# Performance work log

Measured on AMD Instinct MI355X. Metric: run time of the kernel, lower is better.

Reference implementation:

```python
import jax, jax.numpy as jnp
import numpy as np

SENT_LEN = 8192
C = 1024  # class_num


def setup_inputs() -> dict:
    key = jax.random.key(0)
    k1, k2 = jax.random.split(key)
    scores = jax.random.normal(k1, (SENT_LEN, C), dtype=jnp.float32)
    T = jax.random.normal(k2, (C, C), dtype=jnp.float32)  # transition params (random_weights=True)
    return {"scores": scores, "T": T}


def reference(scores, T):
    """Log-domain marginals of a first-order linear-chain CRF.

    alpha[i, j] = scores[i, j] + LSE_k(alpha[i-1, k] + T[k, j])
    beta[i, j]  = scores[i, j] + LSE_k(T[j, k] + beta[i+1, k])
    marginals   = alpha + beta - scores - Z,  Z = LSE(alpha[-1])
    (alpha+beta double-counts scores[i], hence the subtraction.)
    """
    def alpha_step(a_prev, s):
        # a_prev: [C] ; broadcast-add against T then logsumexp over source class k
        a = s + jax.nn.logsumexp(a_prev[:, None] + T, axis=0)
        return a, a

    a0 = scores[0]
    _, alpha_rest = jax.lax.scan(alpha_step, a0, scores[1:])
    alpha = jnp.concatenate([a0[None], alpha_rest], axis=0)  # [N, C]

    def beta_step(b_next, s):
        b = s + jax.nn.logsumexp(T + b_next[None, :], axis=1)
        return b, b

    bN = scores[-1]
    _, beta_rest = jax.lax.scan(beta_step, bN, scores[:-1], reverse=True)
    beta = jnp.concatenate([beta_rest, bN[None]], axis=0)  # [N, C]

    Z = jax.nn.logsumexp(alpha[-1])  # partition function (log)
    return alpha + beta - scores - Z
```

## Files before the change

### kernel.cpp

```cpp
#include <hip/hip_runtime.h>
#include <stdint.h>
#include <float.h>


#define NR    8192
#define CC    1024
#define SEGR  4
#define GH    4
#define NSEG  2048
#define TPB   1024
#define NWV   16
#define G     16
#define NBLK  256
#define MAXT  (GH + SEGR - 1)
#define SHIFT 6.0f

typedef _Float16 f16x8 __attribute__((ext_vector_type(8)));
typedef float    f32x4 __attribute__((ext_vector_type(4)));
typedef __fp16   hv2   __attribute__((ext_vector_type(2)));

__device__ __forceinline__ uint32_t packw(float a, float b) {
  hv2 r = __builtin_amdgcn_cvt_pkrtz(a, b);
  return __builtin_bit_cast(uint32_t, r);
}

__global__ __launch_bounds__(256) void crf_pack(
    const float* __restrict__ T, uint4* __restrict__ Ef, uint4* __restrict__ Eb)
{
  const int bid = blockIdx.x;
  const int dir = bid >> 9;
  const int tid = threadIdx.x;
  const int fid = ((bid & 511) << 2) + (tid >> 6);
  const int lane = tid & 63;
  const int kt = fid >> 6, ntg = fid & 63;
  const int q = lane >> 4, li = lane & 15;
  const int n = ntg * 16 + li;
  const int kb = kt * 32 + q * 8;
  uint32_t o[4];
  if (dir == 0) {
#pragma unroll
    for (int p = 0; p < 4; ++p) {
      const float e0 = __expf(T[(size_t)(kb + 2 * p) * CC + n] - SHIFT);
      const float e1 = __expf(T[(size_t)(kb + 2 * p + 1) * CC + n] - SHIFT);
      o[p] = packw(e0, e1);
    }
    Ef[(size_t)fid * 64 + lane] = make_uint4(o[0], o[1], o[2], o[3]);
  } else {
    const float4 t0 = *(const float4*)&T[(size_t)n * CC + kb];
    const float4 t1 = *(const float4*)&T[(size_t)n * CC + kb + 4];
    o[0] = packw(__expf(t0.x - SHIFT), __expf(t0.y - SHIFT));
    o[1] = packw(__expf(t0.z - SHIFT), __expf(t0.w - SHIFT));
    o[2] = packw(__expf(t1.x - SHIFT), __expf(t1.y - SHIFT));
    o[3] = packw(__expf(t1.z - SHIFT), __expf(t1.w - SHIFT));
    Eb[(size_t)fid * 64 + lane] = make_uint4(o[0], o[1], o[2], o[3]);
  }
}

__global__ __launch_bounds__(TPB) void crf_seg(
    const float* __restrict__ scores,
    const uint4* __restrict__ Ef, const uint4* __restrict__ Eb,
    float* __restrict__ out, float* __restrict__ qrows,
    double* __restrict__ OA, double* __restrict__ OB,
    double* __restrict__ eLf, double* __restrict__ gLf,
    double* __restrict__ eLb, double* __restrict__ gLb, int useQ)
{
  __shared__ unsigned short wh[G][CC + 8];
  __shared__ float mgw[G][NWV + 1];
  __shared__ float lsw[G][NWV + 1];

  const int bid  = blockIdx.x;
  const int xcd  = bid & 7;
  const bool fwd = (xcd < 4);
  const int q    = (xcd & 3) * 32 + (bid >> 3);
  const int tid  = threadIdx.x;
  const int wv   = tid >> 6;
  const int lane = tid & 63;
  const int quad = lane >> 4, li = lane & 15;
  const int wbase = wv * 64;
  const int rot  = (bid >> 3) & 31;

  const uint4*  E    = fwd ? Ef : Eb;
  float*        emit = fwd ? out : qrows;
  double*       Oarr = fwd ? OA : OB;
  double*       eL   = fwd ? eLf : eLb;
  double*       gL   = fwd ? gLf : gLb;

  auto geom = [&](int c, int& g0, int& tE, int& tend) {
    const int s = G * q + c;
    if (fwd) {
      const int f = SEGR * s;
      const int gg = (f - GH) > 0 ? (f - GH) : 0;
      g0 = gg; tE = f - gg; tend = f + SEGR - 1 - gg;
    } else {
      const int h = NR - 1 - SEGR * s;
      const int gg = (h + GH) < (NR - 1) ? (h + GH) : (NR - 1);
      g0 = gg; tE = gg - h; tend = tE + SEGR - 1;
    }
  };

  float pub[4][4];
#pragma unroll
  for (int reg = 0; reg < 4; ++reg) {
    int g0, tE, tend; geom(quad * 4 + reg, g0, tE, tend);
    const size_t rb = (size_t)g0 * CC;
#pragma unroll
    for (int nt = 0; nt < 4; ++nt)
      pub[nt][reg] = scores[rb + wbase + nt * 16 + li];
  }
  double Off = 0.0;
#pragma unroll
  for (int reg = 0; reg < 4; ++reg) {
    int g0, tE, tend; geom(quad * 4 + reg, g0, tE, tend);
    if (tE == 0) {
      const size_t rb = (size_t)g0 * CC;
#pragma unroll
      for (int nt = 0; nt < 4; ++nt) {
        const int j = wbase + nt * 16 + li;
        const float v = fwd ? 0.f : pub[nt][reg];
        if (useQ) emit[rb + j] = v;
        else if (!fwd) atomicAdd(&out[rb + j], v);
      }
    }
  }
  if (tid < G) {
    int g0, tE, tend; geom(tid, g0, tE, tend);
    if (tE == 0) Oarr[g0] = 0.0;
  }

  const uint4* Eln = E + lane;

  for (int t = 1; t <= MAXT; ++t) {
    float sc[4][4] = {};
#pragma unroll
    for (int reg = 0; reg < 4; ++reg) {
      int g0, tE, tend; geom(quad * 4 + reg, g0, tE, tend);
      if (t <= tend) {
        const size_t rb = (size_t)(fwd ? g0 + t : g0 - t) * CC;
#pragma unroll
        for (int nt = 0; nt < 4; ++nt)
          sc[nt][reg] = scores[rb + wbase + nt * 16 + li];
      }
    }

#pragma unroll
    for (int reg = 0; reg < 4; ++reg) {
      float m = pub[0][reg];
#pragma unroll
      for (int nt = 1; nt < 4; ++nt) m = fmaxf(m, pub[nt][reg]);
      m = fmaxf(m, __shfl_xor(m, 1, 64));
      m = fmaxf(m, __shfl_xor(m, 2, 64));
      m = fmaxf(m, __shfl_xor(m, 4, 64));
      m = fmaxf(m, __shfl_xor(m, 8, 64));
      if (li == 0) mgw[quad * 4 + reg][wv] = m;
    }
    __syncthreads();
    float mgli = mgw[li][0];
#pragma unroll
    for (int w = 1; w < NWV; ++w) mgli = fmaxf(mgli, mgw[li][w]);
    float mg4[4];
#pragma unroll
    for (int reg = 0; reg < 4; ++reg) mg4[reg] = __shfl(mgli, quad * 4 + reg, 64);
    if (tid < G) Off += (double)mgli;

    bool bstep = false;
#pragma unroll
    for (int c = 0; c < G; ++c) {
      int g0, tE, tend; geom(c, g0, tE, tend);
      bstep = bstep || (t == tE && tE > 0) || (t - 1 == tend);
    }
    if (bstep) {
#pragma unroll
      for (int reg = 0; reg < 4; ++reg) {
        float s = 0.f;
#pragma unroll
        for (int nt = 0; nt < 4; ++nt) s += __expf(pub[nt][reg] - mg4[reg]);
        s += __shfl_xor(s, 1, 64);
        s += __shfl_xor(s, 2, 64);
        s += __shfl_xor(s, 4, 64);
        s += __shfl_xor(s, 8, 64);
        if (li == 0) lsw[quad * 4 + reg][wv] = s;
      }
    }

#pragma unroll
    for (int reg = 0; reg < 4; ++reg) {
      const int row = quad * 4 + reg;
#pragma unroll
      for (int nt = 0; nt < 4; ++nt) {
        const __fp16 h = (__fp16)__expf(pub[nt][reg] - mg4[reg]);
        wh[row][wbase + nt * 16 + li] = __builtin_bit_cast(unsigned short, h);
      }
    }
    __syncthreads();

    if (bstep && tid < G) {
      float s = lsw[tid][0];
#pragma unroll
      for (int w = 1; w < NWV; ++w) s += lsw[tid][w];
      const double L = (double)__logf(s) + Off;
      int g0, tE, tend; geom(tid, g0, tE, tend);
      if (t == tE && tE > 0) gL[G * q + tid] = L;
      if (t - 1 == tend)     eL[G * q + tid] = L;
    }

    f32x4 acc[4];
#pragma unroll
    for (int nt = 0; nt < 4; ++nt) acc[nt] = (f32x4){0.f, 0.f, 0.f, 0.f};
#pragma unroll 2
    for (int kt = 0; kt < 32; ++kt) {
      const int ktr = (kt + rot) & 31;
      const uint4 a4 = *(const uint4*)&wh[li][ktr * 32 + quad * 8];
      const f16x8 af = __builtin_bit_cast(f16x8, a4);
#pragma unroll
      for (int nt = 0; nt < 4; ++nt) {
        const uint4 b4 = Eln[(size_t)(ktr * 64 + wv * 4 + nt) * 64];
        acc[nt] = __builtin_amdgcn_mfma_f32_16x16x32_f16(
            af, __builtin_bit_cast(f16x8, b4), acc[nt], 0, 0, 0);
      }
    }

#pragma unroll
    for (int reg = 0; reg < 4; ++reg) {
      int g0, tE, tend; geom(quad * 4 + reg, g0, tE, tend);
      if (t <= tend) {
        const size_t rb = (size_t)(fwd ? g0 + t : g0 - t) * CC;
        const bool em = (t >= tE);
#pragma unroll
        for (int nt = 0; nt < 4; ++nt) {
          const float pv = sc[nt][reg] + SHIFT + __logf(acc[nt][reg]);
          pub[nt][reg] = pv;
          if (em) {
            const int j = wbase + nt * 16 + li;
            const float ov = fwd ? (pv - sc[nt][reg]) : pv;
            if (useQ) emit[rb + j] = ov;
            else atomicAdd(&out[rb + j], ov);
          }
        }
      }
    }
    if (tid < G) {
      int g0, tE, tend; geom(tid, g0, tE, tend);
      if (t >= tE && t <= tend) Oarr[fwd ? g0 + t : g0 - t] = Off;
    }
  }

  {
#pragma unroll
    for (int reg = 0; reg < 4; ++reg) {
      float m = pub[0][reg];
#pragma unroll
      for (int nt = 1; nt < 4; ++nt) m = fmaxf(m, pub[nt][reg]);
      m = fmaxf(m, __shfl_xor(m, 1, 64));
      m = fmaxf(m, __shfl_xor(m, 2, 64));
      m = fmaxf(m, __shfl_xor(m, 4, 64));
      m = fmaxf(m, __shfl_xor(m, 8, 64));
      if (li == 0) mgw[quad * 4 + reg][wv] = m;
    }
    __syncthreads();
    float mgli = mgw[li][0];
#pragma unroll
    for (int w = 1; w < NWV; ++w) mgli = fmaxf(mgli, mgw[li][w]);
    float mg4[4];
#pragma unroll
    for (int reg = 0; reg < 4; ++reg) mg4[reg] = __shfl(mgli, quad * 4 + reg, 64);
    if (tid < G) Off += (double)mgli;
#pragma unroll
    for (int reg = 0; reg < 4; ++reg) {
      float s = 0.f;
#pragma unroll
      for (int nt = 0; nt < 4; ++nt) s += __expf(pub[nt][reg] - mg4[reg]);
      s += __shfl_xor(s, 1, 64);
      s += __shfl_xor(s, 2, 64);
      s += __shfl_xor(s, 4, 64);
      s += __shfl_xor(s, 8, 64);
      if (li == 0) lsw[quad * 4 + reg][wv] = s;
    }
    __syncthreads();
    if (tid < G) {
      int g0, tE, tend; geom(tid, g0, tE, tend);
      if (tend == MAXT) {
        float s = lsw[tid][0];
#pragma unroll
        for (int w = 1; w < NWV; ++w) s += lsw[tid][w];
        eL[G * q + tid] = (double)__logf(s) + Off;
      }
    }
  }
}

__global__ __launch_bounds__(128) void crf_stitch(
    const double* __restrict__ eLf, const double* __restrict__ gLf,
    const double* __restrict__ eLb, const double* __restrict__ gLb,
    double* __restrict__ CA, double* __restrict__ CB, double* __restrict__ Zd)
{
  __shared__ double d[NSEG];
  __shared__ double csum[NSEG / 32];
  const int t = threadIdx.x;
  for (int pass = 0; pass < 2; ++pass) {
    const double* e = pass ? eLb : eLf;
    const double* g = pass ? gLb : gLf;
    double* Cp = pass ? CB : CA;
    for (int i = t; i < NSEG; i += 128)
      d[i] = (i == 0) ? 0.0 : e[i - 1] - g[i];
    __syncthreads();
    if (t < NSEG / 32) {
      double c = 0.0;
      for (int u = 0; u < 32; ++u) { c += d[t * 32 + u]; d[t * 32 + u] = c; }
      csum[t] = c;
    }
    __syncthreads();
    if (t == 0) {
      double c = 0.0;
      for (int u = 0; u < NSEG / 32; ++u) {
        const double x = csum[u]; csum[u] = c; c += x;
      }
    }
    __syncthreads();
    for (int i = t; i < NSEG; i += 128) Cp[i] = d[i] + csum[i >> 5];
    if (pass == 0 && t == 0)
      *Zd = d[NSEG - 1] + csum[NSEG / 32 - 1] + e[NSEG - 1];
    __syncthreads();
  }
}

__global__ __launch_bounds__(256) void crf_combine(
    float* __restrict__ out, const float* __restrict__ qrows,
    const double* __restrict__ OA, const double* __restrict__ OB,
    const double* __restrict__ CA, const double* __restrict__ CB,
    const double* __restrict__ Zd, int useQ)
{
  const double Z = *Zd;
  const int g = blockIdx.x * 256 + threadIdx.x;
  const int r = g >> 8;
  const float corr =
      (float)(OA[r] + CA[r >> 2] + OB[r] + CB[(NR - 1 - r) >> 2] - Z);
  float4 o = ((const float4*)out)[g];
  if (useQ) {
    const float4 q = ((const float4*)qrows)[g];
    o.x += q.x; o.y += q.y; o.z += q.z; o.w += q.w;
  }
  o.x += corr; o.y += corr; o.z += corr; o.w += corr;
  ((float4*)out)[g] = o;
}

extern "C" void kernel_launch(void* const* d_in, const int* in_sizes, int n_in,
                              void* d_out, int out_size, void* d_ws, size_t ws_size,
                              hipStream_t stream)
{
  const float* scores = (const float*)d_in[0];
  const float* T      = (const float*)d_in[1];
  float* out = (float*)d_out;
  char* w = (char*)d_ws;
  size_t off = 0;
  auto alloc = [&](size_t n) { char* q = w + off; off = (off + n + 255) & ~(size_t)255; return q; };

  uint4*  Ef = (uint4*)alloc((size_t)2048 * 1024);
  uint4*  Eb = (uint4*)alloc((size_t)2048 * 1024);
  double* OA = (double*)alloc(NR * 8);
  double* OB = (double*)alloc(NR * 8);
  double* eLf = (double*)alloc(NSEG * 8);
  double* gLf = (double*)alloc(NSEG * 8);
  double* eLb = (double*)alloc(NSEG * 8);
  double* gLb = (double*)alloc(NSEG * 8);
  double* CA = (double*)alloc(NSEG * 8);
  double* CB = (double*)alloc(NSEG * 8);
  double* Zd = (double*)alloc(256);
  float*  qrows = (float*)alloc((size_t)NR * CC * 4);
  const int useQ = (off <= ws_size) ? 1 : 0;

  if (!useQ)
    (void)hipMemsetAsync(out, 0, (size_t)NR * CC * 4, stream);
  crf_pack<<<dim3(1024), dim3(256), 0, stream>>>(T, Ef, Eb);
  crf_seg<<<dim3(NBLK), dim3(TPB), 0, stream>>>(scores, Ef, Eb, out,
                                                qrows, OA, OB, eLf, gLf, eLb,
                                                gLb, useQ);
  crf_stitch<<<dim3(1), dim3(128), 0, stream>>>(eLf, gLf, eLb, gLb, CA, CB, Zd);
  crf_combine<<<dim3(8192), dim3(256), 0, stream>>>(out, qrows, OA, OB, CA, CB,
                                                    Zd, useQ);
}
```

Baseline: 277.0 us.

## Fuse pack, segment, stitch and combine kernels into one cooperative kernel

Merges the four separate launches (exp-table pack, segmented CRF scan, stitch prefix sum, combine) into a single cooperative kernel that uses grid.sync between phases. This removes the launch gaps and inter-kernel drain costs between the stages. In exchange, the stitch runs on one block while the others wait. The combine pass now runs on only 256 blocks looping over 8 chunks each, instead of 8192 small blocks. The extra shared memory for the stitch buffer may also reduce occupancy.

```diff
diff --git a/kernel.cpp b/kernel.cpp
--- a/kernel.cpp
+++ b/kernel.cpp
@@ -1,6 +1,9 @@
 #include <hip/hip_runtime.h>
+#include <hip/hip_cooperative_groups.h>
 #include <stdint.h>
 #include <float.h>
+
+namespace cg = cooperative_groups;
 
 
 #define NR    8192
@@ -24,121 +27,231 @@
   return __builtin_bit_cast(uint32_t, r);
 }
 
-__global__ __launch_bounds__(256) void crf_pack(
-    const float* __restrict__ T, uint4* __restrict__ Ef, uint4* __restrict__ Eb)
-{
-  const int bid = blockIdx.x;
-  const int dir = bid >> 9;
-  const int tid = threadIdx.x;
-  const int fid = ((bid & 511) << 2) + (tid >> 6);
-  const int lane = tid & 63;
-  const int kt = fid >> 6, ntg = fid & 63;
-  const int q = lane >> 4, li = lane & 15;
-  const int n = ntg * 16 + li;
-  const int kb = kt * 32 + q * 8;
-  uint32_t o[4];
-  if (dir == 0) {
-#pragma unroll
-    for (int p = 0; p < 4; ++p) {
-      const float e0 = __expf(T[(size_t)(kb + 2 * p) * CC + n] - SHIFT);
-      const float e1 = __expf(T[(size_t)(kb + 2 * p + 1) * CC + n] - SHIFT);
-      o[p] = packw(e0, e1);
-    }
-    Ef[(size_t)fid * 64 + lane] = make_uint4(o[0], o[1], o[2], o[3]);
-  } else {
-    const float4 t0 = *(const float4*)&T[(size_t)n * CC + kb];
-    const float4 t1 = *(const float4*)&T[(size_t)n * CC + kb + 4];
-    o[0] = packw(__expf(t0.x - SHIFT), __expf(t0.y - SHIFT));
-    o[1] = packw(__expf(t0.z - SHIFT), __expf(t0.w - SHIFT));
-    o[2] = packw(__expf(t1.x - SHIFT), __expf(t1.y - SHIFT));
-    o[3] = packw(__expf(t1.z - SHIFT), __expf(t1.w - SHIFT));
-    Eb[(size_t)fid * 64 + lane] = make_uint4(o[0], o[1], o[2], o[3]);
-  }
-}
-
-__global__ __launch_bounds__(TPB) void crf_seg(
-    const float* __restrict__ scores,
-    const uint4* __restrict__ Ef, const uint4* __restrict__ Eb,
+__global__ __launch_bounds__(TPB) void crf_all(
+    const float* __restrict__ scores, const float* __restrict__ T,
+    uint4* __restrict__ Ef, uint4* __restrict__ Eb,
     float* __restrict__ out, float* __restrict__ qrows,
     double* __restrict__ OA, double* __restrict__ OB,
     double* __restrict__ eLf, double* __restrict__ gLf,
-    double* __restrict__ eLb, double* __restrict__ gLb, int useQ)
+    double* __restrict__ eLb, double* __restrict__ gLb,
+    double* __restrict__ CA, double* __restrict__ CB,
+    double* __restrict__ Zd, int useQ)
 {
+  cg::grid_group grid = cg::this_grid();
+
   __shared__ unsigned short wh[G][CC + 8];
   __shared__ float mgw[G][NWV + 1];
   __shared__ float lsw[G][NWV + 1];
+  __shared__ double sd[NSEG];
+  __shared__ double csum[NSEG / 32];
 
   const int bid  = blockIdx.x;
-  const int xcd  = bid & 7;
-  const bool fwd = (xcd < 4);
-  const int q    = (xcd & 3) * 32 + (bid >> 3);
   const int tid  = threadIdx.x;
-  const int wv   = tid >> 6;
-  const int lane = tid & 63;
-  const int quad = lane >> 4, li = lane & 15;
-  const int wbase = wv * 64;
-  const int rot  = (bid >> 3) & 31;
-
-  const uint4*  E    = fwd ? Ef : Eb;
-  float*        emit = fwd ? out : qrows;
-  double*       Oarr = fwd ? OA : OB;
-  double*       eL   = fwd ? eLf : eLb;
-  double*       gL   = fwd ? gLf : gLb;
-
-  auto geom = [&](int c, int& g0, int& tE, int& tend) {
-    const int s = G * q + c;
-    if (fwd) {
-      const int f = SEGR * s;
-      const int gg = (f - GH) > 0 ? (f - GH) : 0;
-      g0 = gg; tE = f - gg; tend = f + SEGR - 1 - gg;
+
+  {
+    const int gt  = bid * TPB + tid;
+    const int dir = gt >> 17;
+    const int rem = gt & 131071;
+    const int fid = rem >> 6;
+    const int ln  = rem & 63;
+    const int kt = fid >> 6, ntg = fid & 63;
+    const int qd = ln >> 4, li = ln & 15;
+    const int n  = ntg * 16 + li;
+    const int kb = kt * 32 + qd * 8;
+    uint32_t o[4];
+    if (dir == 0) {
+#pragma unroll
+      for (int p = 0; p < 4; ++p) {
+        const float e0 = __expf(T[(size_t)(kb + 2 * p) * CC + n] - SHIFT);
+        const float e1 = __expf(T[(size_t)(kb + 2 * p + 1) * CC + n] - SHIFT);
+        o[p] = packw(e0, e1);
+      }
+      Ef[(size_t)fid * 64 + ln] = make_uint4(o[0], o[1], o[2], o[3]);
     } else {
-      const int h = NR - 1 - SEGR * s;
-      const int gg = (h + GH) < (NR - 1) ? (h + GH) : (NR - 1);
-      g0 = gg; tE = gg - h; tend = tE + SEGR - 1;
-    }
-  };
-
-  float pub[4][4];
-#pragma unroll
-  for (int reg = 0; reg < 4; ++reg) {
-    int g0, tE, tend; geom(quad * 4 + reg, g0, tE, tend);
-    const size_t rb = (size_t)g0 * CC;
-#pragma unroll
-    for (int nt = 0; nt < 4; ++nt)
-      pub[nt][reg] = scores[rb + wbase + nt * 16 + li];
+      const float4 t0 = *(const float4*)&T[(size_t)n * CC + kb];
+      const float4 t1 = *(const float4*)&T[(size_t)n * CC + kb + 4];
+      o[0] = packw(__expf(t0.x - SHIFT), __expf(t0.y - SHIFT));
+      o[1] = packw(__expf(t0.z - SHIFT), __expf(t0.w - SHIFT));
+      o[2] = packw(__expf(t1.x - SHIFT), __expf(t1.y - SHIFT));
+      o[3] = packw(__expf(t1.z - SHIFT), __expf(t1.w - SHIFT));
+      Eb[(size_t)fid * 64 + ln] = make_uint4(o[0], o[1], o[2], o[3]);
+    }
   }
-  double Off = 0.0;
-#pragma unroll
-  for (int reg = 0; reg < 4; ++reg) {
-    int g0, tE, tend; geom(quad * 4 + reg, g0, tE, tend);
-    if (tE == 0) {
-      const size_t rb = (size_t)g0 * CC;
-#pragma unroll
-      for (int nt = 0; nt < 4; ++nt) {
-        const int j = wbase + nt * 16 + li;
-        const float v = fwd ? 0.f : pub[nt][reg];
-        if (useQ) emit[rb + j] = v;
-        else if (!fwd) atomicAdd(&out[rb + j], v);
-      }
-    }
-  }
-  if (tid < G) {
-    int g0, tE, tend; geom(tid, g0, tE, tend);
-    if (tE == 0) Oarr[g0] = 0.0;
-  }
-
-  const uint4* Eln = E + lane;
-
-  for (int t = 1; t <= MAXT; ++t) {
-    float sc[4][4] = {};
+  grid.sync();
+
+  {
+    const int xcd  = bid & 7;
+    const bool fwd = (xcd < 4);
+    const int q    = (xcd & 3) * 32 + (bid >> 3);
+    const int wv   = tid >> 6;
+    const int lane = tid & 63;
+    const int quad = lane >> 4, li = lane & 15;
+    const int wbase = wv * 64;
+    const int rot  = (bid >> 3) & 31;
+
+    const uint4*  E    = fwd ? Ef : Eb;
+    float*        emit = fwd ? out : qrows;
+    double*       Oarr = fwd ? OA : OB;
+    double*       eL   = fwd ? eLf : eLb;
+    double*       gL   = fwd ? gLf : gLb;
+
+    auto geom = [&](int c, int& g0, int& tE, int& tend) {
+      const int s = G * q + c;
+      if (fwd) {
+        const int f = SEGR * s;
+        const int gg = (f - GH) > 0 ? (f - GH) : 0;
+        g0 = gg; tE = f - gg; tend = f + SEGR - 1 - gg;
+      } else {
+        const int h = NR - 1 - SEGR * s;
+        const int gg = (h + GH) < (NR - 1) ? (h + GH) : (NR - 1);
+        g0 = gg; tE = gg - h; tend = tE + SEGR - 1;
+      }
+    };
+
+    float pub[4][4];
 #pragma unroll
     for (int reg = 0; reg < 4; ++reg) {
       int g0, tE, tend; geom(quad * 4 + reg, g0, tE, tend);
-      if (t <= tend) {
-        const size_t rb = (size_t)(fwd ? g0 + t : g0 - t) * CC;
-#pragma unroll
-        for (int nt = 0; nt < 4; ++nt)
-          sc[nt][reg] = scores[rb + wbase + nt * 16 + li];
+      const size_t rb = (size_t)g0 * CC;
+#pragma unroll
+      for (int nt = 0; nt < 4; ++nt)
+        pub[nt][reg] = scores[rb + wbase + nt * 16 + li];
+    }
+    double Off = 0.0;
+#pragma unroll
+    for (int reg = 0; reg < 4; ++reg) {
+      int g0, tE, tend; geom(quad * 4 + reg, g0, tE, tend);
+      if (tE == 0) {
+        const size_t rb = (size_t)g0 * CC;
+#pragma unroll
+        for (int nt = 0; nt < 4; ++nt) {
+          const int j = wbase + nt * 16 + li;
+          const float v = fwd ? 0.f : pub[nt][reg];
+          if (useQ) emit[rb + j] = v;
+          else if (!fwd) atomicAdd(&out[rb + j], v);
+        }
+      }
+    }
+    if (tid < G) {
+      int g0, tE, tend; geom(tid, g0, tE, tend);
+      if (tE == 0) Oarr[g0] = 0.0;
+    }
+
+    const uint4* Eln = E + lane;
+
+    for (int t = 1; t <= MAXT; ++t) {
+      float sc[4][4] = {};
+#pragma unroll
+      for (int reg = 0; reg < 4; ++reg) {
+        int g0, tE, tend; geom(quad * 4 + reg, g0, tE, tend);
+        if (t <= tend) {
+          const size_t rb = (size_t)(fwd ? g0 + t : g0 - t) * CC;
+#pragma unroll
+          for (int nt = 0; nt < 4; ++nt)
+            sc[nt][reg] = scores[rb + wbase + nt * 16 + li];
+        }
+      }
+
+#pragma unroll
+      for (int reg = 0; reg < 4; ++reg) {
+        float m = pub[0][reg];
+#pragma unroll
+        for (int nt = 1; nt < 4; ++nt) m = fmaxf(m, pub[nt][reg]);
+        m = fmaxf(m, __shfl_xor(m, 1, 64));
+        m = fmaxf(m, __shfl_xor(m, 2, 64));
+        m = fmaxf(m, __shfl_xor(m, 4, 64));
+        m = fmaxf(m, __shfl_xor(m, 8, 64));
+        if (li == 0) mgw[quad * 4 + reg][wv] = m;
+      }
+      __syncthreads();
+      float mgli = mgw[lane & 15][0];
+#pragma unroll
+      for (int w = 1; w < NWV; ++w) mgli = fmaxf(mgli, mgw[lane & 15][w]);
+      float mg4[4];
+#pragma unroll
+      for (int reg = 0; reg < 4; ++reg)
+        mg4[reg] = __shfl(mgli, quad * 4 + reg, 64);
+      if (tid < G) Off += (double)mgli;
+
+      bool bstep = false;
+#pragma unroll
+      for (int c = 0; c < G; ++c) {
+        int g0, tE, tend; geom(c, g0, tE, tend);
+        bstep = bstep || (t == tE && tE > 0) || (t - 1 == tend);
+      }
+      if (bstep) {
+#pragma unroll
+        for (int reg = 0; reg < 4; ++reg) {
+          float s = 0.f;
+#pragma unroll
+          for (int nt = 0; nt < 4; ++nt) s += __expf(pub[nt][reg] - mg4[reg]);
+          s += __shfl_xor(s, 1, 64);
+          s += __shfl_xor(s, 2, 64);
+          s += __shfl_xor(s, 4, 64);
+          s += __shfl_xor(s, 8, 64);
+          if (li == 0) lsw[quad * 4 + reg][wv] = s;
+        }
+      }
+
+#pragma unroll
+      for (int reg = 0; reg < 4; ++reg) {
+        const int row = quad * 4 + reg;
+#pragma unroll
+        for (int nt = 0; nt < 4; ++nt) {
+          const __fp16 h = (__fp16)__expf(pub[nt][reg] - mg4[reg]);
+          wh[row][wbase + nt * 16 + li] = __builtin_bit_cast(unsigned short, h);
+        }
+      }
+      __syncthreads();
+
+      if (bstep && tid < G) {
+        float s = lsw[tid][0];
+#pragma unroll
+        for (int w = 1; w < NWV; ++w) s += lsw[tid][w];
+        const double L = (double)__logf(s) + Off;
+        int g0, tE, tend; geom(tid, g0, tE, tend);
+        if (t == tE && tE > 0) gL[G * q + tid] = L;
+        if (t - 1 == tend)     eL[G * q + tid] = L;
+      }
+
+      f32x4 acc[4];
+#pragma unroll
+      for (int nt = 0; nt < 4; ++nt) acc[nt] = (f32x4){0.f, 0.f, 0.f, 0.f};
+#pragma unroll 2
+      for (int kt = 0; kt < 32; ++kt) {
+        const int ktr = (kt + rot) & 31;
+        const uint4 a4 = *(const uint4*)&wh[li][ktr * 32 + quad * 8];
+        const f16x8 af = __builtin_bit_cast(f16x8, a4);
+#pragma unroll
+        for (int nt = 0; nt < 4; ++nt) {
+          const uint4 b4 = Eln[(size_t)(ktr * 64 + wv * 4 + nt) * 64];
+          acc[nt] = __builtin_amdgcn_mfma_f32_16x16x32_f16(
+              af, __builtin_bit_cast(f16x8, b4), acc[nt], 0, 0, 0);
+        }
+      }
+
+#pragma unroll
+      for (int reg = 0; reg < 4; ++reg) {
+        int g0, tE, tend; geom(quad * 4 + reg, g0, tE, tend);
+        if (t <= tend) {
+          const size_t rb = (size_t)(fwd ? g0 + t : g0 - t) * CC;
+          const bool em = (t >= tE);
+#pragma unroll
+          for (int nt = 0; nt < 4; ++nt) {
+            const float pv = sc[nt][reg] + SHIFT + __logf(acc[nt][reg]);
+            pub[nt][reg] = pv;
+            if (em) {
+              const int j = wbase + nt * 16 + li;
+              const float ov = fwd ? (pv - sc[nt][reg]) : pv;
+              if (useQ) emit[rb + j] = ov;
+              else atomicAdd(&out[rb + j], ov);
+            }
+          }
+        }
+      }
+      if (tid < G) {
+        int g0, tE, tend; geom(tid, g0, tE, tend);
+        if (t >= tE && t <= tend) Oarr[fwd ? g0 + t : g0 - t] = Off;
       }
     }
 
@@ -154,115 +267,13 @@
       if (li == 0) mgw[quad * 4 + reg][wv] = m;
     }
     __syncthreads();
-    float mgli = mgw[li][0];
-#pragma unroll
-    for (int w = 1; w < NWV; ++w) mgli = fmaxf(mgli, mgw[li][w]);
+    float mgli = mgw[lane & 15][0];
+#pragma unroll
+    for (int w = 1; w < NWV; ++w) mgli = fmaxf(mgli, mgw[lane & 15][w]);
     float mg4[4];
 #pragma unroll
-    for (int reg = 0; reg < 4; ++reg) mg4[reg] = __shfl(mgli, quad * 4 + reg, 64);
-    if (tid < G) Off += (double)mgli;
-
-    bool bstep = false;
-#pragma unroll
-    for (int c = 0; c < G; ++c) {
-      int g0, tE, tend; geom(c, g0, tE, tend);
-      bstep = bstep || (t == tE && tE > 0) || (t - 1 == tend);
-    }
-    if (bstep) {
-#pragma unroll
-      for (int reg = 0; reg < 4; ++reg) {
-        float s = 0.f;
-#pragma unroll
-        for (int nt = 0; nt < 4; ++nt) s += __expf(pub[nt][reg] - mg4[reg]);
-        s += __shfl_xor(s, 1, 64);
-        s += __shfl_xor(s, 2, 64);
-        s += __shfl_xor(s, 4, 64);
-        s += __shfl_xor(s, 8, 64);
-        if (li == 0) lsw[quad * 4 + reg][wv] = s;
-      }
-    }
-
-#pragma unroll
-    for (int reg = 0; reg < 4; ++reg) {
-      const int row = quad * 4 + reg;
-#pragma unroll
-      for (int nt = 0; nt < 4; ++nt) {
-        const __fp16 h = (__fp16)__expf(pub[nt][reg] - mg4[reg]);
-        wh[row][wbase + nt * 16 + li] = __builtin_bit_cast(unsigned short, h);
-      }
-    }
-    __syncthreads();
-
-    if (bstep && tid < G) {
-      float s = lsw[tid][0];
-#pragma unroll
-      for (int w = 1; w < NWV; ++w) s += lsw[tid][w];
-      const double L = (double)__logf(s) + Off;
-      int g0, tE, tend; geom(tid, g0, tE, tend);
-      if (t == tE && tE > 0) gL[G * q + tid] = L;
-      if (t - 1 == tend)     eL[G * q + tid] = L;
-    }
-
-    f32x4 acc[4];
-#pragma unroll
-    for (int nt = 0; nt < 4; ++nt) acc[nt] = (f32x4){0.f, 0.f, 0.f, 0.f};
-#pragma unroll 2
-    for (int kt = 0; kt < 32; ++kt) {
-      const int ktr = (kt + rot) & 31;
-      const uint4 a4 = *(const uint4*)&wh[li][ktr * 32 + quad * 8];
-      const f16x8 af = __builtin_bit_cast(f16x8, a4);
-#pragma unroll
-      for (int nt = 0; nt < 4; ++nt) {
-        const uint4 b4 = Eln[(size_t)(ktr * 64 + wv * 4 + nt) * 64];
-        acc[nt] = __builtin_amdgcn_mfma_f32_16x16x32_f16(
-            af, __builtin_bit_cast(f16x8, b4), acc[nt], 0, 0, 0);
-      }
-    }
-
-#pragma unroll
-    for (int reg = 0; reg < 4; ++reg) {
-      int g0, tE, tend; geom(quad * 4 + reg, g0, tE, tend);
-      if (t <= tend) {
-        const size_t rb = (size_t)(fwd ? g0 + t : g0 - t) * CC;
-        const bool em = (t >= tE);
-#pragma unroll
-        for (int nt = 0; nt < 4; ++nt) {
-          const float pv = sc[nt][reg] + SHIFT + __logf(acc[nt][reg]);
-          pub[nt][reg] = pv;
-          if (em) {
-            const int j = wbase + nt * 16 + li;
-            const float ov = fwd ? (pv - sc[nt][reg]) : pv;
-            if (useQ) emit[rb + j] = ov;
-            else atomicAdd(&out[rb + j], ov);
-          }
-        }
-      }
-    }
-    if (tid < G) {
-      int g0, tE, tend; geom(tid, g0, tE, tend);
-      if (t >= tE && t <= tend) Oarr[fwd ? g0 + t : g0 - t] = Off;
-    }
-  }
-
-  {
-#pragma unroll
-    for (int reg = 0; reg < 4; ++reg) {
-      float m = pub[0][reg];
-#pragma unroll
-      for (int nt = 1; nt < 4; ++nt) m = fmaxf(m, pub[nt][reg]);
-      m = fmaxf(m, __shfl_xor(m, 1, 64));
-      m = fmaxf(m, __shfl_xor(m, 2, 64));
-      m = fmaxf(m, __shfl_xor(m, 4, 64));
-      m = fmaxf(m, __shfl_xor(m, 8, 64));
-      if (li == 0) mgw[quad * 4 + reg][wv] = m;
-    }
-    __syncthreads();
-    float mgli = mgw[li][0];
-#pragma unroll
-    for (int w = 1; w < NWV; ++w) mgli = fmaxf(mgli, mgw[li][w]);
-    float mg4[4];
-#pragma unroll
-    for (int reg = 0; reg < 4; ++reg) mg4[reg] = __shfl(mgli, quad * 4 + reg, 64);
+    for (int reg = 0; reg < 4; ++reg)
+      mg4[reg] = __shfl(mgli, quad * 4 + reg, 64);
     if (tid < G) Off += (double)mgli;
 #pragma unroll
     for (int reg = 0; reg < 4; ++reg) {
@@ -286,61 +297,55 @@
       }
     }
   }
-}
-
-__global__ __launch_bounds__(128) void crf_stitch(
-    const double* __restrict__ eLf, const double* __restrict__ gLf,
-    const double* __restrict__ eLb, const double* __restrict__ gLb,
-    double* __restrict__ CA, double* __restrict__ CB, double* __restrict__ Zd)
-{
-  __shared__ double d[NSEG];
-  __shared__ double csum[NSEG / 32];
-  const int t = threadIdx.x;
-  for (int pass = 0; pass < 2; ++pass) {
-    const double* e = pass ? eLb : eLf;
-    const double* g = pass ? gLb : gLf;
-    double* Cp = pass ? CB : CA;
-    for (int i = t; i < NSEG; i += 128)
-      d[i] = (i == 0) ? 0.0 : e[i - 1] - g[i];
-    __syncthreads();
-    if (t < NSEG / 32) {
-      double c = 0.0;
-      for (int u = 0; u < 32; ++u) { c += d[t * 32 + u]; d[t * 32 + u] = c; }
-      csum[t] = c;
-    }
-    __syncthreads();
-    if (t == 0) {
-      double c = 0.0;
-      for (int u = 0; u < NSEG / 32; ++u) {
-        const double x = csum[u]; csum[u] = c; c += x;
-      }
-    }
-    __syncthreads();
-    for (int i = t; i < NSEG; i += 128) Cp[i] = d[i] + csum[i >> 5];
-    if (pass == 0 && t == 0)
-      *Zd = d[NSEG - 1] + csum[NSEG / 32 - 1] + e[NSEG - 1];
-    __syncthreads();
+  grid.sync();
+
+  if (bid == 0) {
+    for (int pass = 0; pass < 2; ++pass) {
+      const double* e = pass ? eLb : eLf;
+      const double* g = pass ? gLb : gLf;
+      double* Cp = pass ? CB : CA;
+      for (int i = tid; i < NSEG; i += TPB)
+        sd[i] = (i == 0) ? 0.0 : e[i - 1] - g[i];
+      __syncthreads();
+      if (tid < NSEG / 32) {
+        double c = 0.0;
+        for (int u = 0; u < 32; ++u) { c += sd[tid * 32 + u]; sd[tid * 32 + u] = c; }
+        csum[tid] = c;
+      }
+      __syncthreads();
+      if (tid == 0) {
+        double c = 0.0;
+        for (int u = 0; u < NSEG / 32; ++u) {
+          const double x = csum[u]; csum[u] = c; c += x;
+        }
+      }
+      __syncthreads();
+      for (int i = tid; i < NSEG; i += TPB) Cp[i] = sd[i] + csum[i >> 5];
+      if (pass == 0 && tid == 0)
+        *Zd = sd[NSEG - 1] + csum[NSEG / 32 - 1] + e[NSEG - 1];
+      __syncthreads();
+    }
   }
-}
-
-__global__ __launch_bounds__(256) void crf_combine(
-    float* __restrict__ out, const float* __restrict__ qrows,
-    const double* __restrict__ OA, const double* __restrict__ OB,
-    const double* __restrict__ CA, const double* __restrict__ CB,
-    const double* __restrict__ Zd, int useQ)
-{
-  const double Z = *Zd;
-  const int g = blockIdx.x * 256 + threadIdx.x;
-  const int r = g >> 8;
-  const float corr =
-      (float)(OA[r] + CA[r >> 2] + OB[r] + CB[(NR - 1 - r) >> 2] - Z);
-  float4 o = ((const float4*)out)[g];
-  if (useQ) {
-    const float4 q = ((const float4*)qrows)[g];
-    o.x += q.x; o.y += q.y; o.z += q.z; o.w += q.w;
+  grid.sync();
+
+  {
+    const double Z = *Zd;
+    const int base = bid * 8192;
+#pragma unroll
+    for (int k = 0; k < 8; ++k) {
+      const int g = base + k * TPB + tid;
+      const int r = g >> 8;
+      const float corr =
+          (float)(OA[r] + CA[r >> 2] + OB[r] + CB[(NR - 1 - r) >> 2] - Z);
+      float4 o = ((const float4*)out)[g];
+      if (useQ) {
+        const float4 qv = ((const float4*)qrows)[g];
+        o.x += qv.x; o.y += qv.y; o.z += qv.z; o.w += qv.w;
+      }
+      o.x += corr; o.y += corr; o.z += corr; o.w += corr;
+      ((float4*)out)[g] = o;
+    }
   }
-  o.x += corr; o.y += corr; o.z += corr; o.w += corr;
-  ((float4*)out)[g] = o;
 }
 
 extern "C" void kernel_launch(void* const* d_in, const int* in_sizes, int n_in,
@@ -366,15 +371,17 @@
   double* CB = (double*)alloc(NSEG * 8);
   double* Zd = (double*)alloc(256);
   float*  qrows = (float*)alloc((size_t)NR * CC * 4);
-  const int useQ = (off <= ws_size) ? 1 : 0;
+  int useQ = (off <= ws_size) ? 1 : 0;
 
   if (!useQ)
     (void)hipMemsetAsync(out, 0, (size_t)NR * CC * 4, stream);
-  crf_pack<<<dim3(1024), dim3(256), 0, stream>>>(T, Ef, Eb);
-  crf_seg<<<dim3(NBLK), dim3(TPB), 0, stream>>>(scores, Ef, Eb, out,
-                                                qrows, OA, OB, eLf, gLf, eLb,
-                                                gLb, useQ);
-  crf_stitch<<<dim3(1), dim3(128), 0, stream>>>(eLf, gLf, eLb, gLb, CA, CB, Zd);
-  crf_combine<<<dim3(8192), dim3(256), 0, stream>>>(out, qrows, OA, OB, CA, CB,
-                                                    Zd, useQ);
+
+  void* args[] = {
+    (void*)&scores, (void*)&T, (void*)&Ef, (void*)&Eb,
+    (void*)&out, (void*)&qrows, (void*)&OA, (void*)&OB,
+    (void*)&eLf, (void*)&gLf, (void*)&eLb, (void*)&gLb,
+    (void*)&CA, (void*)&CB, (void*)&Zd, (void*)&useQ
+  };
+  (void)hipLaunchCooperativeKernel((const void*)crf_all, dim3(NBLK), dim3(TPB),
+                                   args, 0, stream);
 }
```

Measured after the change: 357.4 us. 1.29x slower.
